# Optimization experiments

Measured on AMD Instinct MI355X. Metric: run time of the kernel, lower is better.

The kernel has to match this reference:

```python
import jax, jax.numpy as jnp
import numpy as np

B, N, DM, H = 2, 512, 1024, 16  # batch, seq, d_model, n_heads
DEPTHS = [1, 2, 4, 8]
LAM = 0.1  # lambda_distance


def setup_inputs() -> dict:
    key = jax.random.key(0)
    ks = jax.random.split(key, 2 + 5 * len(DEPTHS))
    inp = {
        "x": jax.random.normal(ks[0], (B, N, DM), jnp.float32),
        "depth_logits": jax.random.normal(ks[1], (len(DEPTHS),), jnp.float32),
    }
    j = 2
    for i, D in enumerate(DEPTHS):
        ds = DM // D
        r = max(1, D // 4)
        inp[f"pe{i}"] = jax.random.normal(ks[j], (N, D, ds), jnp.float32) * 0.02; j += 1
        inp[f"wqkv{i}"] = jax.random.normal(ks[j], (D, ds, 3 * ds), jnp.float32) / np.sqrt(ds); j += 1
        inp[f"wo{i}"] = jax.random.normal(ks[j], (DM, DM), jnp.float32) / np.sqrt(DM); j += 1
        inp[f"fu{i}"] = jax.random.normal(ks[j], (D, r), jnp.float32) / np.sqrt(r); j += 1
        inp[f"fv{i}"] = jax.random.normal(ks[j], (r, D), jnp.float32); j += 1
    return inp


def _ring_bias(n, lam, dtype):
    # toroidal (circular) distance bias on the sequence ring, normalized by N/2
    idx = jnp.arange(n)
    diff = jnp.abs(idx[:, None] - idx[None, :])
    ring = jnp.minimum(diff, n - diff).astype(dtype)
    return -lam * ring * (2.0 / n)  # [N, N]


def _toroidal_branch(x, pe, wqkv, wo, fu, fv):
    # x: [B, N, DM]; pe: [N, D, ds]; wqkv: [D, ds, 3ds]; wo: [DM, DM]; fu@fv: [D, D]
    b, n, dm = x.shape
    d_depth, ds, _ = wqkv.shape
    hd = ds // H
    xs = x.reshape(b, n, d_depth, ds) + pe[None]          # [B, N, D, ds]
    qkv = jnp.einsum('bnds,dse->bnde', xs, wqkv)          # per-depth-slice projection
    q, k, v = jnp.split(qkv, 3, axis=-1)
    q = q.reshape(b, n, d_depth, H, hd)
    k = k.reshape(b, n, d_depth, H, hd)
    v = v.reshape(b, n, d_depth, H, hd)
    bias = _ring_bias(n, LAM, x.dtype)
    scores = jnp.einsum('bndhe,bmdhe->bdhnm', q, k) / jnp.sqrt(jnp.asarray(hd, x.dtype))
    attn = jax.nn.softmax(scores + bias, axis=-1)          # [B, D, H, N, N]
    o = jnp.einsum('bdhnm,bmdhe->bndhe', attn, v).reshape(b, n, d_depth, ds)
    mix = fu @ fv                                          # low-rank depth fusion [D, D]
    fused = jnp.einsum('df,bnfs->bnds', mix, o).reshape(b, n, dm)
    return fused @ wo


def _forward(x, depth_logits, pe0, wqkv0, wo0, fu0, fv0, pe1, wqkv1, wo1, fu1, fv1,
             pe2, wqkv2, wo2, fu2, fv2, pe3, wqkv3, wo3, fu3, fv3):
    # inference-mode depth selection: hard one-hot at argmax (all branches still computed)
    w = jax.nn.one_hot(jnp.argmax(depth_logits), depth_logits.shape[0], dtype=x.dtype)
    params = [(pe0, wqkv0, wo0, fu0, fv0), (pe1, wqkv1, wo1, fu1, fv1),
              (pe2, wqkv2, wo2, fu2, fv2), (pe3, wqkv3, wo3, fu3, fv3)]
    out = jnp.zeros_like(x)
    for i, p in enumerate(params):
        out = out + w[i] * _toroidal_branch(x, *p)
    return out


def reference(x, depth_logits, pe0, wqkv0, wo0, fu0, fv0, pe1, wqkv1, wo1, fu1, fv1,
              pe2, wqkv2, wo2, fu2, fv2, pe3, wqkv3, wo3, fu3, fv3):
    return _forward(x, depth_logits, pe0, wqkv0, wo0, fu0, fv0, pe1, wqkv1, wo1, fu1, fv1,
                    pe2, wqkv2, wo2, fu2, fv2, pe3, wqkv3, wo3, fu3, fv3)
```

## Files before the change

### kernel.cpp

```cpp
#include <hip/hip_runtime.h>

#define B_   2
#define N_   512
#define DM_  1024
#define H_   16
#define LAM_ 0.1f

typedef __attribute__((ext_vector_type(8))) short bf16x8;
typedef __attribute__((ext_vector_type(4))) float f32x4;
typedef unsigned short ush;
struct ush4 { ush x, y, z, w; };

__device__ inline ush f2bf(float v) {
    union { float f; unsigned u; } c; c.f = v;
    unsigned r = c.u + 0x7FFF + ((c.u >> 16) & 1);
    return (ush)(r >> 16);
}
__device__ inline float bf2f(ush b) {
    union { float f; unsigned u; } c; c.u = ((unsigned)b) << 16; return c.f;
}
__device__ inline f32x4 mfma16(bf16x8 a, bf16x8 b, f32x4 c) {
    return __builtin_amdgcn_mfma_f32_16x16x32_bf16(a, b, c, 0, 0, 0);
}

__global__ void k_select(const float* __restrict__ logits, int* __restrict__ sel) {
    if (threadIdx.x == 0) {
        float best = logits[0]; int bi = 0;
        for (int i = 1; i < 4; ++i) { float v = logits[i]; if (v > best) { best = v; bi = i; } }
        *sel = bi;
    }
}

template<int D>
__device__ void prep_w_body(size_t i, const float* __restrict__ w,
                            ush* __restrict__ wh, ush* __restrict__ wl) {
    constexpr int ds = DM_ / D;
    constexpr size_t TOT = (size_t)D * ds * 3 * ds;
    if (i >= TOT) return;
    const int per = ds * 3 * ds;
    const int d = (int)(i / per), rem = (int)(i % per);
    const int s = rem / (3 * ds), e = rem % (3 * ds);
    const float v = w[i];
    const size_t o = (size_t)d * 3 * ds * ds + (size_t)e * ds + s;
    const ush h = f2bf(v);
    wh[o] = h; wl[o] = f2bf(v - bf2f(h));
}
__global__ __launch_bounds__(256) void k_prep(
        const int* __restrict__ sel, const float* __restrict__ x,
        const float* __restrict__ pe0, const float* __restrict__ pe1,
        const float* __restrict__ pe2, const float* __restrict__ pe3,
        const float* __restrict__ w0, const float* __restrict__ w1,
        const float* __restrict__ w2, const float* __restrict__ w3,
        const float* __restrict__ wo0, const float* __restrict__ wo1,
        const float* __restrict__ wo2, const float* __restrict__ wo3,
        ush* __restrict__ xh, ush* __restrict__ xl,
        ush* __restrict__ wqh, ush* __restrict__ wql,
        ush* __restrict__ woh, ush* __restrict__ wol) {
    const int s = *sel;
    const int bid = blockIdx.x, tid = threadIdx.x;
    if (bid < 4096) {
        const float* pe = (s == 0) ? pe0 : (s == 1) ? pe1 : (s == 2) ? pe2 : pe3;
        const size_t i = (size_t)bid * 256 + tid;
        const float v = x[i] + pe[i % ((size_t)N_ * DM_)];
        const ush h = f2bf(v);
        xh[i] = h; xl[i] = f2bf(v - bf2f(h));
    } else if (bid < 16384) {
        const size_t i = (size_t)(bid - 4096) * 256 + tid;
        switch (s) {
            case 0: prep_w_body<1>(i, w0, wqh, wql); break;
            case 1: prep_w_body<2>(i, w1, wqh, wql); break;
            case 2: prep_w_body<4>(i, w2, wqh, wql); break;
            case 3: prep_w_body<8>(i, w3, wqh, wql); break;
        }
    } else {
        const float* w = (s == 0) ? wo0 : (s == 1) ? wo1 : (s == 2) ? wo2 : wo3;
        const size_t i = (size_t)(bid - 16384) * 256 + tid;
        const int k = (int)(i / DM_), j = (int)(i % DM_);
        const float v = w[i];
        const size_t o = (size_t)j * DM_ + k;
        const ush h = f2bf(v);
        woh[o] = h; wol[o] = f2bf(v - bf2f(h));
    }
}

template<int KD>
__device__ void gemm_core(const ush* __restrict__ Ah, const ush* __restrict__ Al, int lda,
                          const ush* __restrict__ Bh, const ush* __restrict__ Bl, int ldb,
                          int row0, int col0, int tid, ush* lds, f32x4 acc[2][2]) {
    ush* lAh = lds; ush* lAl = lds + 2560; ush* lBh = lds + 5120; ush* lBl = lds + 7680;
    const int srow = tid >> 2, scg = tid & 3;
    const int lane = tid & 63, w = tid >> 6;
    const int wm = w >> 1, wn = w & 1;
    const int lr = lane & 15, lb = lane >> 4;

    for (int k0 = 0; k0 < KD; k0 += 32) {
        *(bf16x8*)&lAh[srow * 40 + scg * 8] =
            *(const bf16x8*)&Ah[(size_t)(row0 + srow) * lda + k0 + scg * 8];
        *(bf16x8*)&lAl[srow * 40 + scg * 8] =
            *(const bf16x8*)&Al[(size_t)(row0 + srow) * lda + k0 + scg * 8];
        *(bf16x8*)&lBh[srow * 40 + scg * 8] =
            *(const bf16x8*)&Bh[(size_t)(col0 + srow) * ldb + k0 + scg * 8];
        *(bf16x8*)&lBl[srow * 40 + scg * 8] =
            *(const bf16x8*)&Bl[(size_t)(col0 + srow) * ldb + k0 + scg * 8];
        __syncthreads();
        bf16x8 ah[2], al[2], bh[2], bl[2];
        #pragma unroll
        for (int mg = 0; mg < 2; ++mg) {
            const int r = wm * 32 + mg * 16 + lr;
            ah[mg] = *(const bf16x8*)&lAh[r * 40 + lb * 8];
            al[mg] = *(const bf16x8*)&lAl[r * 40 + lb * 8];
        }
        #pragma unroll
        for (int ng = 0; ng < 2; ++ng) {
            const int r = wn * 32 + ng * 16 + lr;
            bh[ng] = *(const bf16x8*)&lBh[r * 40 + lb * 8];
            bl[ng] = *(const bf16x8*)&lBl[r * 40 + lb * 8];
        }
        #pragma unroll
        for (int mg = 0; mg < 2; ++mg)
            #pragma unroll
            for (int ng = 0; ng < 2; ++ng) {
                acc[mg][ng] = mfma16(ah[mg], bh[ng], acc[mg][ng]);
                acc[mg][ng] = mfma16(al[mg], bh[ng], acc[mg][ng]);
                acc[mg][ng] = mfma16(ah[mg], bl[ng], acc[mg][ng]);
            }
        __syncthreads();
    }
}

template<int D>
__device__ void qkv_body(int bid, int tid,
                         const ush* __restrict__ xh, const ush* __restrict__ xl,
                         const ush* __restrict__ wh, const ush* __restrict__ wl,
                         ush* __restrict__ Qh, ush* __restrict__ Ql,
                         ush* __restrict__ Kh, ush* __restrict__ Kl,
                         ush* __restrict__ Vth, ush* __restrict__ Vtl, ush* lds) {
    constexpr int ds = DM_ / D;
    constexpr int hd = ds / H_;
    constexpr int nx = 3 * ds / 64;
    const int bx = bid % nx, by = (bid / nx) & 7, bz = bid / (nx * 8);
    const int b = bz / D, d = bz % D;
    const int row0 = by * 64, col0 = bx * 64;

    f32x4 acc[2][2] = {};
    gemm_core<ds>(xh + (size_t)b * N_ * DM_ + d * ds, xl + (size_t)b * N_ * DM_ + d * ds, DM_,
                  wh + (size_t)d * 3 * ds * ds, wl + (size_t)d * 3 * ds * ds, ds,
                  row0, col0, tid, lds, acc);

    const int lane = tid & 63, w = tid >> 6;
    const int wm = w >> 1, wn = w & 1;
    const int lr = lane & 15, lb = lane >> 4;
    #pragma unroll
    for (int mg = 0; mg < 2; ++mg)
        #pragma unroll
        for (int ng = 0; ng < 2; ++ng) {
            const int n0 = row0 + wm * 32 + mg * 16 + lb * 4;
            const int e  = col0 + wn * 32 + ng * 16 + lr;
            const int part = e / ds, ep = e % ds;
            const int h = ep / hd, t = ep % hd;
            const size_t head = ((size_t)b * D + d) * H_ + h;
            if (part == 2) {
                ush4 h4, l4;
                const float v0 = acc[mg][ng][0], v1 = acc[mg][ng][1];
                const float v2 = acc[mg][ng][2], v3 = acc[mg][ng][3];
                h4.x = f2bf(v0); l4.x = f2bf(v0 - bf2f(h4.x));
                h4.y = f2bf(v1); l4.y = f2bf(v1 - bf2f(h4.y));
                h4.z = f2bf(v2); l4.z = f2bf(v2 - bf2f(h4.z));
                h4.w = f2bf(v3); l4.w = f2bf(v3 - bf2f(h4.w));
                const size_t o = (head * hd + t) * N_ + n0;
                *(ush4*)&Vth[o] = h4;
                *(ush4*)&Vtl[o] = l4;
            } else {
                #pragma unroll
                for (int i = 0; i < 4; ++i) {
                    const size_t o = (head * N_ + n0 + i) * hd + t;
                    const float v = acc[mg][ng][i];
                    const ush hh = f2bf(v), ll = f2bf(v - bf2f(hh));
                    if (part == 0) { Qh[o] = hh; Ql[o] = ll; }
                    else           { Kh[o] = hh; Kl[o] = ll; }
                }
            }
        }
}
__global__ __launch_bounds__(256) void k_qkv(
        const int* __restrict__ sel,
        const ush* __restrict__ xh, const ush* __restrict__ xl,
        const ush* __restrict__ wh, const ush* __restrict__ wl,
        ush* __restrict__ Qh, ush* __restrict__ Ql,
        ush* __restrict__ Kh, ush* __restrict__ Kl,
        ush* __restrict__ Vth, ush* __restrict__ Vtl) {
    __shared__ ush lds[4 * 2560];
    const int bid = blockIdx.x, tid = threadIdx.x;
    switch (*sel) {
        case 0: qkv_body<1>(bid, tid, xh, xl, wh, wl, Qh, Ql, Kh, Kl, Vth, Vtl, lds); break;
        case 1: qkv_body<2>(bid, tid, xh, xl, wh, wl, Qh, Ql, Kh, Kl, Vth, Vtl, lds); break;
        case 2: qkv_body<4>(bid, tid, xh, xl, wh, wl, Qh, Ql, Kh, Kl, Vth, Vtl, lds); break;
        case 3: qkv_body<8>(bid, tid, xh, xl, wh, wl, Qh, Ql, Kh, Kl, Vth, Vtl, lds); break;
    }
}

template<int D>
__device__ void attn_body(int bid, int tid,
        const ush* __restrict__ Qh, const ush* __restrict__ Ql,
        const ush* __restrict__ Kh, const ush* __restrict__ Kl,
        const ush* __restrict__ Vth, const ush* __restrict__ Vtl,
        float* __restrict__ O, ush* P, float* redm, float* redl) {
    constexpr int ds = DM_ / D, hd = ds / H_;
    constexpr int CH = (hd >= 64) ? 2 : 1;
    constexpr int NT = (hd >= 16) ? hd / 16 : 1;
    constexpr int NHEAD = B_ * D * H_;
    constexpr int NB = NHEAD * 32;
    if (bid >= NB) return;
    const int bidr = (bid & 7) * (NB / 8) + (bid >> 3);
    const int head = bidr >> 5, qt = bidr & 31;
    const int h = head % H_, d = (head / H_) % D, b = head / (H_ * D);
    const int q0 = qt * 16;
    const size_t hb = (size_t)head * N_ * hd;
    const int lane = tid & 63, wk = tid >> 6;
    const int lr = lane & 15, lb = lane >> 4;
    const float L2E = 1.44269504f;
    const float SC  = rsqrtf((float)hd) * L2E;
    const float RB2 = LAM_ * (2.0f / N_) * L2E;
    const bf16x8 z8 = {0, 0, 0, 0, 0, 0, 0, 0};

    bf16x8 qah[CH], qal[CH];
    #pragma unroll
    for (int c = 0; c < CH; ++c) {
        const int k0 = c * 32 + lb * 8;
        bf16x8 vh = z8, vl = z8;
        if (k0 < hd) {
            const size_t o = hb + (size_t)(q0 + lr) * hd + k0;
            vh = *(const bf16x8*)&Qh[o];
            vl = *(const bf16x8*)&Ql[o];
        }
        qah[c] = vh; qal[c] = vl;
    }

    f32x4 s[8];
    #pragma unroll
    for (int t = 0; t < 8; ++t) {
        const int kj0 = wk * 128 + t * 16;
        f32x4 acc = {0.f, 0.f, 0.f, 0.f};
        #pragma unroll
        for (int c = 0; c < CH; ++c) {
            const int k0 = c * 32 + lb * 8;
            bf16x8 kh8 = z8, kl8 = z8;
            if (k0 < hd) {
                const size_t o = hb + (size_t)(kj0 + lr) * hd + k0;
                kh8 = *(const bf16x8*)&Kh[o];
                kl8 = *(const bf16x8*)&Kl[o];
            }
            acc = mfma16(qah[c], kh8, acc);
            acc = mfma16(qal[c], kh8, acc);
            acc = mfma16(qah[c], kl8, acc);
        }
        s[t] = acc;
    }

    float m4[4] = {-1e30f, -1e30f, -1e30f, -1e30f};
    #pragma unroll
    for (int t = 0; t < 8; ++t) {
        const int col = wk * 128 + t * 16 + lr;
        #pragma unroll
        for (int i = 0; i < 4; ++i) {
            const int rn = q0 + lb * 4 + i;
            int dd = rn - col; dd = dd < 0 ? -dd : dd;
            const int ring = (dd < N_ - dd) ? dd : (N_ - dd);
            const float v = s[t][i] * SC - RB2 * (float)ring;
            s[t][i] = v;
            m4[i] = fmaxf(m4[i], v);
        }
    }
    #pragma unroll
    for (int i = 0; i < 4; ++i) {
        m4[i] = fmaxf(m4[i], __shfl_xor(m4[i], 1));
        m4[i] = fmaxf(m4[i], __shfl_xor(m4[i], 2));
        m4[i] = fmaxf(m4[i], __shfl_xor(m4[i], 4));
        m4[i] = fmaxf(m4[i], __shfl_xor(m4[i], 8));
    }
    if (lr == 0) {
        #pragma unroll
        for (int i = 0; i < 4; ++i) redm[wk * 16 + lb * 4 + i] = m4[i];
    }

    ush* Pw = P + wk * 2048;
    float ls[4] = {0.f, 0.f, 0.f, 0.f};
    #pragma unroll
    for (int t = 0; t < 8; t += 2) {
        #pragma unroll
        for (int i = 0; i < 4; ++i) {
            const int row = lb * 4 + i;
            const float pe = exp2f(s[t][i] - m4[i]);
            const float po = exp2f(s[t + 1][i] - m4[i]);
            unsigned pk;
            asm("v_cvt_pk_bf16_f32 %0, %1, %2" : "=v"(pk) : "v"(pe), "v"(po));
            union { unsigned u; float f; } clo, chi;
            clo.u = pk << 16;
            chi.u = pk & 0xffff0000u;
            ls[i] += clo.f + chi.f;
            const int swz = (row & 7) << 4;
            const int offe = ((row << 8) + ((t * 16 + lr) << 1)) ^ swz;
            const int offo = ((row << 8) + (((t + 1) * 16 + lr) << 1)) ^ swz;
            *(ush*)((char*)Pw + offe) = (ush)pk;
            *(ush*)((char*)Pw + offo) = (ush)(pk >> 16);
        }
    }
    #pragma unroll
    for (int i = 0; i < 4; ++i) {
        ls[i] += __shfl_xor(ls[i], 1);
        ls[i] += __shfl_xor(ls[i], 2);
        ls[i] += __shfl_xor(ls[i], 4);
        ls[i] += __shfl_xor(ls[i], 8);
    }
    if (lr == 0) {
        #pragma unroll
        for (int i = 0; i < 4; ++i) redl[wk * 16 + lb * 4 + i] = ls[i];
    }

    f32x4 acc2[NT];
    #pragma unroll
    for (int tt = 0; tt < NT; ++tt) acc2[tt] = (f32x4){0.f, 0.f, 0.f, 0.f};
    #pragma unroll
    for (int jc = 0; jc < 4; ++jc) {
        int poff = ((lr << 8) + ((jc * 32 + lb * 8) << 1)) ^ ((lr & 7) << 4);
        const bf16x8 pa = *(const bf16x8*)((const char*)Pw + poff);
        #pragma unroll
        for (int tt = 0; tt < NT; ++tt) {
            const size_t o = hb + (size_t)(tt * 16 + lr) * N_ + wk * 128 + jc * 32 + lb * 8;
            const bf16x8 vh8 = *(const bf16x8*)&Vth[o];
            const bf16x8 vl8 = *(const bf16x8*)&Vtl[o];
            acc2[tt] = mfma16(pa, vh8, acc2[tt]);
            acc2[tt] = mfma16(pa, vl8, acc2[tt]);
        }
    }

    __syncthreads();
    float* res = (float*)P;
    if (wk != 0) {
        #pragma unroll
        for (int tt = 0; tt < NT; ++tt)
            #pragma unroll
            for (int i = 0; i < 4; ++i)
                res[((wk - 1) * NT + tt) * 256 + i * 64 + lane] = acc2[tt][i];
    }
    __syncthreads();
    if (wk == 0) {
        float scw[4][4], linv[4];
        #pragma unroll
        for (int i = 0; i < 4; ++i) {
            const int r = lb * 4 + i;
            const float mw0 = redm[r], mw1 = redm[16 + r];
            const float mw2 = redm[32 + r], mw3 = redm[48 + r];
            const float m = fmaxf(fmaxf(mw0, mw1), fmaxf(mw2, mw3));
            scw[i][0] = exp2f(mw0 - m); scw[i][1] = exp2f(mw1 - m);
            scw[i][2] = exp2f(mw2 - m); scw[i][3] = exp2f(mw3 - m);
            const float l = redl[r] * scw[i][0] + redl[16 + r] * scw[i][1]
                          + redl[32 + r] * scw[i][2] + redl[48 + r] * scw[i][3];
            linv[i] = 1.0f / l;
        }
        #pragma unroll
        for (int tt = 0; tt < NT; ++tt)
            #pragma unroll
            for (int i = 0; i < 4; ++i) {
                const float o = acc2[tt][i] * scw[i][0]
                    + res[(0 * NT + tt) * 256 + i * 64 + lane] * scw[i][1]
                    + res[(1 * NT + tt) * 256 + i * 64 + lane] * scw[i][2]
                    + res[(2 * NT + tt) * 256 + i * 64 + lane] * scw[i][3];
                const int rn = q0 + lb * 4 + i;
                const int tc = tt * 16 + lr;
                if (tc < hd)
                    O[((size_t)b * N_ + rn) * DM_ + d * ds + h * hd + tc] = o * linv[i];
            }
    }
}
__global__ __launch_bounds__(256) void k_attn(
        const int* __restrict__ sel,
        const ush* __restrict__ Qh, const ush* __restrict__ Ql,
        const ush* __restrict__ Kh, const ush* __restrict__ Kl,
        const ush* __restrict__ Vth, const ush* __restrict__ Vtl,
        float* __restrict__ O) {
    __shared__ __align__(16) ush P[4 * 16 * 128];
    __shared__ float redm[64], redl[64];
    const int bid = blockIdx.x, tid = threadIdx.x;
    switch (*sel) {
        case 0: attn_body<1>(bid, tid, Qh, Ql, Kh, Kl, Vth, Vtl, O, P, redm, redl); break;
        case 1: attn_body<2>(bid, tid, Qh, Ql, Kh, Kl, Vth, Vtl, O, P, redm, redl); break;
        case 2: attn_body<4>(bid, tid, Qh, Ql, Kh, Kl, Vth, Vtl, O, P, redm, redl); break;
        case 3: attn_body<8>(bid, tid, Qh, Ql, Kh, Kl, Vth, Vtl, O, P, redm, redl); break;
    }
}

template<int D>
__device__ void mix_body(int bid, int tid, const float* __restrict__ fu,
                         const float* __restrict__ fv, const float* __restrict__ O,
                         ush* __restrict__ Fh, ush* __restrict__ Fl, float* mixs) {
    constexpr int ds = DM_ / D;
    constexpr int R = (D / 4 > 0) ? (D / 4) : 1;
    if (tid < D * D) {
        const int d = tid / D, f = tid % D;
        float m = 0.f;
        #pragma unroll
        for (int rr = 0; rr < R; ++rr) m += fu[d * R + rr] * fv[rr * D + f];
        mixs[tid] = m;
    }
    __syncthreads();
    const size_t idx = (size_t)bid * 256 + tid;
    const int dm = (int)(idx % DM_);
    const size_t bn = idx / DM_;
    const int d = dm / ds, s0 = dm % ds;
    const float* Ob = O + bn * DM_ + s0;
    float acc = 0.f;
    #pragma unroll
    for (int f = 0; f < D; ++f) acc += mixs[d * D + f] * Ob[(size_t)f * ds];
    const ush hh = f2bf(acc);
    Fh[idx] = hh; Fl[idx] = f2bf(acc - bf2f(hh));
}
__global__ __launch_bounds__(256) void k_mix(
        const int* __restrict__ sel,
        const float* __restrict__ fu0, const float* __restrict__ fv0,
        const float* __restrict__ fu1, const float* __restrict__ fv1,
        const float* __restrict__ fu2, const float* __restrict__ fv2,
        const float* __restrict__ fu3, const float* __restrict__ fv3,
        const float* __restrict__ O, ush* __restrict__ Fh, ush* __restrict__ Fl) {
    __shared__ float mixs[64];
    const int bid = blockIdx.x, tid = threadIdx.x;
    switch (*sel) {
        case 0: mix_body<1>(bid, tid, fu0, fv0, O, Fh, Fl, mixs); break;
        case 1: mix_body<2>(bid, tid, fu1, fv1, O, Fh, Fl, mixs); break;
        case 2: mix_body<4>(bid, tid, fu2, fv2, O, Fh, Fl, mixs); break;
        case 3: mix_body<8>(bid, tid, fu3, fv3, O, Fh, Fl, mixs); break;
    }
}

__global__ __launch_bounds__(256) void k_wo(
        const ush* __restrict__ Fh, const ush* __restrict__ Fl,
        const ush* __restrict__ wh, const ush* __restrict__ wl,
        float* __restrict__ out) {
    __shared__ ush lds[4 * 2560];
    const int tid = threadIdx.x;
    const int bx = blockIdx.x % 16, by = blockIdx.x / 16;
    const int row0 = by * 64, col0 = bx * 64;
    f32x4 acc[2][2] = {};
    gemm_core<DM_>(Fh, Fl, DM_, wh, wl, DM_, row0, col0, tid, lds, acc);
    const int lane = tid & 63, w = tid >> 6;
    const int wm = w >> 1, wn = w & 1;
    const int lr = lane & 15, lb = lane >> 4;
    #pragma unroll
    for (int mg = 0; mg < 2; ++mg)
        #pragma unroll
        for (int ng = 0; ng < 2; ++ng)
            #pragma unroll
            for (int i = 0; i < 4; ++i) {
                const int r = row0 + wm * 32 + mg * 16 + lb * 4 + i;
                const int c = col0 + wn * 32 + ng * 16 + lr;
                out[(size_t)r * DM_ + c] = acc[mg][ng][i];
            }
}

extern "C" void kernel_launch(void* const* d_in, const int* in_sizes, int n_in,
                              void* d_out, int out_size, void* d_ws, size_t ws_size,
                              hipStream_t stream) {
    const float* x      = (const float*)d_in[0];
    const float* logits = (const float*)d_in[1];
    float* out = (float*)d_out;

    char* p = (char*)d_ws;
    int* sel = (int*)p; p += 256;
    const size_t MB = 1024 * 1024;
    ush* Qh = (ush*)p; p += 2 * MB;
    ush* Ql = (ush*)p; p += 2 * MB;
    ush* Kh = (ush*)p; p += 2 * MB;
    ush* Kl = (ush*)p; p += 2 * MB;
    ush* Vth = (ush*)p; p += 2 * MB + 65536;
    ush* Vtl = (ush*)p; p += 2 * MB + 65536;
    float* O = (float*)p; p += 4 * MB;
    ush* xh = (ush*)p; p += 2 * MB;
    ush* xl = (ush*)p; p += 2 * MB;
    ush* wqh = (ush*)p; p += 6 * MB;
    ush* wql = (ush*)p; p += 6 * MB;
    ush* woh = (ush*)p; p += 2 * MB;
    ush* wol = (ush*)p; p += 2 * MB;
    ush* Fh = xh, *Fl = xl;

    k_select<<<1, 64, 0, stream>>>(logits, sel);
    k_prep<<<dim3(20480), dim3(256), 0, stream>>>(
        sel, x,
        (const float*)d_in[2], (const float*)d_in[7],
        (const float*)d_in[12], (const float*)d_in[17],
        (const float*)d_in[3], (const float*)d_in[8],
        (const float*)d_in[13], (const float*)d_in[18],
        (const float*)d_in[4], (const float*)d_in[9],
        (const float*)d_in[14], (const float*)d_in[19],
        xh, xl, wqh, wql, woh, wol);
    k_qkv<<<dim3(768), dim3(256), 0, stream>>>(sel, xh, xl, wqh, wql,
                                               Qh, Ql, Kh, Kl, Vth, Vtl);
    k_attn<<<dim3(8192), dim3(256), 0, stream>>>(sel, Qh, Ql, Kh, Kl, Vth, Vtl, O);
    k_mix<<<dim3(B_ * N_ * DM_ / 256), dim3(256), 0, stream>>>(
        sel,
        (const float*)d_in[5],  (const float*)d_in[6],
        (const float*)d_in[10], (const float*)d_in[11],
        (const float*)d_in[15], (const float*)d_in[16],
        (const float*)d_in[20], (const float*)d_in[21],
        O, Fh, Fl);
    k_wo<<<dim3(256), dim3(256), 0, stream>>>(Fh, Fl, woh, wol, out);
}
```

Before: 109.2 us.

## Tile weight transposes via LDS, drop softmax max pass, retile output GEMM

```diff
diff --git a/kernel.cpp b/kernel.cpp
--- a/kernel.cpp
+++ b/kernel.cpp
@@ -10,6 +10,7 @@
 typedef __attribute__((ext_vector_type(4))) float f32x4;
 typedef unsigned short ush;
 struct ush4 { ush x, y, z, w; };
+struct uint2s { unsigned x, y; };
 
 __device__ inline ush f2bf(float v) {
     union { float f; unsigned u; } c; c.f = v;
@@ -32,18 +33,34 @@
 }
 
 template<int D>
-__device__ void prep_w_body(size_t i, const float* __restrict__ w,
-                            ush* __restrict__ wh, ush* __restrict__ wl) {
+__device__ void prep_wt_tile(int bT, int tid, const float* __restrict__ w,
+                             ush* __restrict__ wh, ush* __restrict__ wl,
+                             float (*lds)[65]) {
     constexpr int ds = DM_ / D;
-    constexpr size_t TOT = (size_t)D * ds * 3 * ds;
-    if (i >= TOT) return;
-    const int per = ds * 3 * ds;
-    const int d = (int)(i / per), rem = (int)(i % per);
-    const int s = rem / (3 * ds), e = rem % (3 * ds);
-    const float v = w[i];
-    const size_t o = (size_t)d * 3 * ds * ds + (size_t)e * ds + s;
-    const ush h = f2bf(v);
-    wh[o] = h; wl[o] = f2bf(v - bf2f(h));
+    constexpr int tpr = 3 * ds / 64;
+    constexpr int tpc = ds / 64;
+    constexpr int tpd = tpr * tpc;
+    if (bT >= D * tpd) return;
+    const int d = bT / tpd, rem = bT % tpd;
+    const int tr = rem / tpr, tc = rem % tpr;
+    const float* src = w + (size_t)d * ds * 3 * ds;
+    ush* dsth = wh + (size_t)d * 3 * ds * ds;
+    ush* dstl = wl + (size_t)d * 3 * ds * ds;
+    const int c = tid & 63, r0 = tid >> 6;
+    #pragma unroll
+    for (int j = 0; j < 16; ++j) {
+        const int r = j * 4 + r0;
+        lds[r][c] = src[(size_t)(tr * 64 + r) * (3 * ds) + tc * 64 + c];
+    }
+    __syncthreads();
+    #pragma unroll
+    for (int j = 0; j < 16; ++j) {
+        const int r = j * 4 + r0;
+        const float v = lds[c][r];
+        const size_t o = (size_t)(tc * 64 + r) * ds + tr * 64 + c;
+        const ush h = f2bf(v);
+        dsth[o] = h; dstl[o] = f2bf(v - bf2f(h));
+    }
 }
 __global__ __launch_bounds__(256) void k_prep(
         const int* __restrict__ sel, const float* __restrict__ x,
@@ -56,30 +73,49 @@
         ush* __restrict__ xh, ush* __restrict__ xl,
         ush* __restrict__ wqh, ush* __restrict__ wql,
         ush* __restrict__ woh, ush* __restrict__ wol) {
+    __shared__ float lds[64][65];
     const int s = *sel;
     const int bid = blockIdx.x, tid = threadIdx.x;
-    if (bid < 4096) {
+    if (bid < 1024) {
         const float* pe = (s == 0) ? pe0 : (s == 1) ? pe1 : (s == 2) ? pe2 : pe3;
-        const size_t i = (size_t)bid * 256 + tid;
-        const float v = x[i] + pe[i % ((size_t)N_ * DM_)];
-        const ush h = f2bf(v);
-        xh[i] = h; xl[i] = f2bf(v - bf2f(h));
-    } else if (bid < 16384) {
-        const size_t i = (size_t)(bid - 4096) * 256 + tid;
+        const size_t i0 = ((size_t)bid * 256 + tid) * 4;
+        const float4 xv = *(const float4*)&x[i0];
+        const float4 pv = *(const float4*)&pe[i0 & ((size_t)N_ * DM_ - 1)];
+        ush4 h4, l4;
+        float v;
+        v = xv.x + pv.x; h4.x = f2bf(v); l4.x = f2bf(v - bf2f(h4.x));
+        v = xv.y + pv.y; h4.y = f2bf(v); l4.y = f2bf(v - bf2f(h4.y));
+        v = xv.z + pv.z; h4.z = f2bf(v); l4.z = f2bf(v - bf2f(h4.z));
+        v = xv.w + pv.w; h4.w = f2bf(v); l4.w = f2bf(v - bf2f(h4.w));
+        *(ush4*)&xh[i0] = h4;
+        *(ush4*)&xl[i0] = l4;
+    } else if (bid < 1792) {
+        const int bT = bid - 1024;
         switch (s) {
-            case 0: prep_w_body<1>(i, w0, wqh, wql); break;
-            case 1: prep_w_body<2>(i, w1, wqh, wql); break;
-            case 2: prep_w_body<4>(i, w2, wqh, wql); break;
-            case 3: prep_w_body<8>(i, w3, wqh, wql); break;
+            case 0: prep_wt_tile<1>(bT, tid, w0, wqh, wql, lds); break;
+            case 1: prep_wt_tile<2>(bT, tid, w1, wqh, wql, lds); break;
+            case 2: prep_wt_tile<4>(bT, tid, w2, wqh, wql, lds); break;
+            case 3: prep_wt_tile<8>(bT, tid, w3, wqh, wql, lds); break;
         }
     } else {
         const float* w = (s == 0) ? wo0 : (s == 1) ? wo1 : (s == 2) ? wo2 : wo3;
-        const size_t i = (size_t)(bid - 16384) * 256 + tid;
-        const int k = (int)(i / DM_), j = (int)(i % DM_);
-        const float v = w[i];
-        const size_t o = (size_t)j * DM_ + k;
-        const ush h = f2bf(v);
-        woh[o] = h; wol[o] = f2bf(v - bf2f(h));
+        const int bT = bid - 1792;
+        const int tr = bT >> 4, tc = bT & 15;
+        const int c = tid & 63, r0 = tid >> 6;
+        #pragma unroll
+        for (int j = 0; j < 16; ++j) {
+            const int r = j * 4 + r0;
+            lds[r][c] = w[(size_t)(tr * 64 + r) * DM_ + tc * 64 + c];
+        }
+        __syncthreads();
+        #pragma unroll
+        for (int j = 0; j < 16; ++j) {
+            const int r = j * 4 + r0;
+            const float v = lds[c][r];
+            const size_t o = (size_t)(tc * 64 + r) * DM_ + tr * 64 + c;
+            const ush h = f2bf(v);
+            woh[o] = h; wol[o] = f2bf(v - bf2f(h));
+        }
     }
 }
 
@@ -204,7 +240,7 @@
         const ush* __restrict__ Qh, const ush* __restrict__ Ql,
         const ush* __restrict__ Kh, const ush* __restrict__ Kl,
         const ush* __restrict__ Vth, const ush* __restrict__ Vtl,
-        float* __restrict__ O, ush* P, float* redm, float* redl) {
+        float* __restrict__ O, ush* P, float* redl) {
     constexpr int ds = DM_ / D, hd = ds / H_;
     constexpr int CH = (hd >= 64) ? 2 : 1;
     constexpr int NT = (hd >= 16) ? hd / 16 : 1;
@@ -250,72 +286,40 @@
                 kh8 = *(const bf16x8*)&Kh[o];
                 kl8 = *(const bf16x8*)&Kl[o];
             }
-            acc = mfma16(qah[c], kh8, acc);
-            acc = mfma16(qal[c], kh8, acc);
-            acc = mfma16(qah[c], kl8, acc);
+            acc = mfma16(kh8, qah[c], acc);
+            acc = mfma16(kl8, qah[c], acc);
+            acc = mfma16(kh8, qal[c], acc);
         }
         s[t] = acc;
     }
 
-    float m4[4] = {-1e30f, -1e30f, -1e30f, -1e30f};
+    ush* Pw = P + wk * 2048;
+    const int q = q0 + lr;
+    float ls = 0.f;
     #pragma unroll
     for (int t = 0; t < 8; ++t) {
-        const int col = wk * 128 + t * 16 + lr;
+        const int kbase = wk * 128 + t * 16 + lb * 4;
+        float p[4];
         #pragma unroll
         for (int i = 0; i < 4; ++i) {
-            const int rn = q0 + lb * 4 + i;
-            int dd = rn - col; dd = dd < 0 ? -dd : dd;
+            int dd = q - (kbase + i); dd = dd < 0 ? -dd : dd;
             const int ring = (dd < N_ - dd) ? dd : (N_ - dd);
-            const float v = s[t][i] * SC - RB2 * (float)ring;
-            s[t][i] = v;
-            m4[i] = fmaxf(m4[i], v);
-        }
-    }
-    #pragma unroll
-    for (int i = 0; i < 4; ++i) {
-        m4[i] = fmaxf(m4[i], __shfl_xor(m4[i], 1));
-        m4[i] = fmaxf(m4[i], __shfl_xor(m4[i], 2));
-        m4[i] = fmaxf(m4[i], __shfl_xor(m4[i], 4));
-        m4[i] = fmaxf(m4[i], __shfl_xor(m4[i], 8));
-    }
-    if (lr == 0) {
-        #pragma unroll
-        for (int i = 0; i < 4; ++i) redm[wk * 16 + lb * 4 + i] = m4[i];
-    }
-
-    ush* Pw = P + wk * 2048;
-    float ls[4] = {0.f, 0.f, 0.f, 0.f};
-    #pragma unroll
-    for (int t = 0; t < 8; t += 2) {
-        #pragma unroll
-        for (int i = 0; i < 4; ++i) {
-            const int row = lb * 4 + i;
-            const float pe = exp2f(s[t][i] - m4[i]);
-            const float po = exp2f(s[t + 1][i] - m4[i]);
-            unsigned pk;
-            asm("v_cvt_pk_bf16_f32 %0, %1, %2" : "=v"(pk) : "v"(pe), "v"(po));
-            union { unsigned u; float f; } clo, chi;
-            clo.u = pk << 16;
-            chi.u = pk & 0xffff0000u;
-            ls[i] += clo.f + chi.f;
-            const int swz = (row & 7) << 4;
-            const int offe = ((row << 8) + ((t * 16 + lr) << 1)) ^ swz;
-            const int offo = ((row << 8) + (((t + 1) * 16 + lr) << 1)) ^ swz;
-            *(ush*)((char*)Pw + offe) = (ush)pk;
-            *(ush*)((char*)Pw + offo) = (ush)(pk >> 16);
-        }
-    }
-    #pragma unroll
-    for (int i = 0; i < 4; ++i) {
-        ls[i] += __shfl_xor(ls[i], 1);
-        ls[i] += __shfl_xor(ls[i], 2);
-        ls[i] += __shfl_xor(ls[i], 4);
-        ls[i] += __shfl_xor(ls[i], 8);
-    }
-    if (lr == 0) {
-        #pragma unroll
-        for (int i = 0; i < 4; ++i) redl[wk * 16 + lb * 4 + i] = ls[i];
-    }
+            p[i] = exp2f(s[t][i] * SC - RB2 * (float)ring);
+        }
+        unsigned pk0, pk1;
+        asm("v_cvt_pk_bf16_f32 %0, %1, %2" : "=v"(pk0) : "v"(p[0]), "v"(p[1]));
+        asm("v_cvt_pk_bf16_f32 %0, %1, %2" : "=v"(pk1) : "v"(p[2]), "v"(p[3]));
+        union { unsigned u; float f; } c0, c1, c2, c3;
+        c0.u = pk0 << 16; c1.u = pk0 & 0xffff0000u;
+        c2.u = pk1 << 16; c3.u = pk1 & 0xffff0000u;
+        ls += (c0.f + c1.f) + (c2.f + c3.f);
+        const int off = ((lr << 8) + ((t * 16 + lb * 4) << 1)) ^ ((lr & 7) << 4);
+        uint2s pv; pv.x = pk0; pv.y = pk1;
+        *(uint2s*)((char*)Pw + off) = pv;
+    }
+    ls += __shfl_xor(ls, 16);
+    ls += __shfl_xor(ls, 32);
+    if (lb == 0) redl[wk * 16 + lr] = ls;
 
     f32x4 acc2[NT];
     #pragma unroll
@@ -345,27 +349,20 @@
     }
     __syncthreads();
     if (wk == 0) {
-        float scw[4][4], linv[4];
+        float linv[4];
         #pragma unroll
         for (int i = 0; i < 4; ++i) {
             const int r = lb * 4 + i;
-            const float mw0 = redm[r], mw1 = redm[16 + r];
-            const float mw2 = redm[32 + r], mw3 = redm[48 + r];
-            const float m = fmaxf(fmaxf(mw0, mw1), fmaxf(mw2, mw3));
-            scw[i][0] = exp2f(mw0 - m); scw[i][1] = exp2f(mw1 - m);
-            scw[i][2] = exp2f(mw2 - m); scw[i][3] = exp2f(mw3 - m);
-            const float l = redl[r] * scw[i][0] + redl[16 + r] * scw[i][1]
-                          + redl[32 + r] * scw[i][2] + redl[48 + r] * scw[i][3];
-            linv[i] = 1.0f / l;
+            linv[i] = 1.0f / (redl[r] + redl[16 + r] + redl[32 + r] + redl[48 + r]);
         }
         #pragma unroll
         for (int tt = 0; tt < NT; ++tt)
             #pragma unroll
             for (int i = 0; i < 4; ++i) {
-                const float o = acc2[tt][i] * scw[i][0]
-                    + res[(0 * NT + tt) * 256 + i * 64 + lane] * scw[i][1]
-                    + res[(1 * NT + tt) * 256 + i * 64 + lane] * scw[i][2]
-                    + res[(2 * NT + tt) * 256 + i * 64 + lane] * scw[i][3];
+                const float o = acc2[tt][i]
+                    + res[(0 * NT + tt) * 256 + i * 64 + lane]
+                    + res[(1 * NT + tt) * 256 + i * 64 + lane]
+                    + res[(2 * NT + tt) * 256 + i * 64 + lane];
                 const int rn = q0 + lb * 4 + i;
                 const int tc = tt * 16 + lr;
                 if (tc < hd)
@@ -380,13 +377,13 @@
         const ush* __restrict__ Vth, const ush* __restrict__ Vtl,
         float* __restrict__ O) {
     __shared__ __align__(16) ush P[4 * 16 * 128];
-    __shared__ float redm[64], redl[64];
+    __shared__ float redl[64];
     const int bid = blockIdx.x, tid = threadIdx.x;
     switch (*sel) {
-        case 0: attn_body<1>(bid, tid, Qh, Ql, Kh, Kl, Vth, Vtl, O, P, redm, redl); break;
-        case 1: attn_body<2>(bid, tid, Qh, Ql, Kh, Kl, Vth, Vtl, O, P, redm, redl); break;
-        case 2: attn_body<4>(bid, tid, Qh, Ql, Kh, Kl, Vth, Vtl, O, P, redm, redl); break;
-        case 3: attn_body<8>(bid, tid, Qh, Ql, Kh, Kl, Vth, Vtl, O, P, redm, redl); break;
+        case 0: attn_body<1>(bid, tid, Qh, Ql, Kh, Kl, Vth, Vtl, O, P, redl); break;
+        case 1: attn_body<2>(bid, tid, Qh, Ql, Kh, Kl, Vth, Vtl, O, P, redl); break;
+        case 2: attn_body<4>(bid, tid, Qh, Ql, Kh, Kl, Vth, Vtl, O, P, redl); break;
+        case 3: attn_body<8>(bid, tid, Qh, Ql, Kh, Kl, Vth, Vtl, O, P, redl); break;
     }
 }
 
@@ -436,25 +433,54 @@
         const ush* __restrict__ Fh, const ush* __restrict__ Fl,
         const ush* __restrict__ wh, const ush* __restrict__ wl,
         float* __restrict__ out) {
-    __shared__ ush lds[4 * 2560];
+    __shared__ ush lA[2][32 * 40];
+    __shared__ ush lB[2][64 * 40];
     const int tid = threadIdx.x;
-    const int bx = blockIdx.x % 16, by = blockIdx.x / 16;
-    const int row0 = by * 64, col0 = bx * 64;
-    f32x4 acc[2][2] = {};
-    gemm_core<DM_>(Fh, Fl, DM_, wh, wl, DM_, row0, col0, tid, lds, acc);
+    const int bx = blockIdx.x & 15, by = blockIdx.x >> 4;
+    const int row0 = by * 32, col0 = bx * 64;
     const int lane = tid & 63, w = tid >> 6;
-    const int wm = w >> 1, wn = w & 1;
+    const int wq = w >> 1, wn = w & 1;
     const int lr = lane & 15, lb = lane >> 4;
-    #pragma unroll
-    for (int mg = 0; mg < 2; ++mg)
-        #pragma unroll
-        for (int ng = 0; ng < 2; ++ng)
-            #pragma unroll
-            for (int i = 0; i < 4; ++i) {
-                const int r = row0 + wm * 32 + mg * 16 + lb * 4 + i;
-                const int c = col0 + wn * 32 + ng * 16 + lr;
-                out[(size_t)r * DM_ + c] = acc[mg][ng][i];
-            }
+    f32x4 acc[2] = {};
+
+    for (int k0 = 0; k0 < DM_; k0 += 32) {
+        {
+            const int half = tid >> 7, t2 = tid & 127;
+            const int srow = t2 >> 2, scg = t2 & 3;
+            const ush* src = half ? Fl : Fh;
+            *(bf16x8*)&lA[half][srow * 40 + scg * 8] =
+                *(const bf16x8*)&src[(size_t)(row0 + srow) * DM_ + k0 + scg * 8];
+        }
+        {
+            const int srow = tid >> 2, scg = tid & 3;
+            *(bf16x8*)&lB[0][srow * 40 + scg * 8] =
+                *(const bf16x8*)&wh[(size_t)(col0 + srow) * DM_ + k0 + scg * 8];
+            *(bf16x8*)&lB[1][srow * 40 + scg * 8] =
+                *(const bf16x8*)&wl[(size_t)(col0 + srow) * DM_ + k0 + scg * 8];
+        }
+        __syncthreads();
+        const int ar = wq * 16 + lr;
+        const bf16x8 ah = *(const bf16x8*)&lA[0][ar * 40 + lb * 8];
+        const bf16x8 al = *(const bf16x8*)&lA[1][ar * 40 + lb * 8];
+        #pragma unroll
+        for (int ng = 0; ng < 2; ++ng) {
+            const int br = wn * 32 + ng * 16 + lr;
+            const bf16x8 bh = *(const bf16x8*)&lB[0][br * 40 + lb * 8];
+            const bf16x8 bl = *(const bf16x8*)&lB[1][br * 40 + lb * 8];
+            acc[ng] = mfma16(ah, bh, acc[ng]);
+            acc[ng] = mfma16(al, bh, acc[ng]);
+            acc[ng] = mfma16(ah, bl, acc[ng]);
+        }
+        __syncthreads();
+    }
+    #pragma unroll
+    for (int ng = 0; ng < 2; ++ng)
+        #pragma unroll
+        for (int i = 0; i < 4; ++i) {
+            const int r = row0 + wq * 16 + lb * 4 + i;
+            const int c = col0 + wn * 32 + ng * 16 + lr;
+            out[(size_t)r * DM_ + c] = acc[ng][i];
+        }
 }
 
 extern "C" void kernel_launch(void* const* d_in, const int* in_sizes, int n_in,
@@ -483,7 +509,7 @@
     ush* Fh = xh, *Fl = xl;
 
     k_select<<<1, 64, 0, stream>>>(logits, sel);
-    k_prep<<<dim3(20480), dim3(256), 0, stream>>>(
+    k_prep<<<dim3(2048), dim3(256), 0, stream>>>(
         sel, x,
         (const float*)d_in[2], (const float*)d_in[7],
         (const float*)d_in[12], (const float*)d_in[17],
@@ -502,5 +528,5 @@
         (const float*)d_in[15], (const float*)d_in[16],
         (const float*)d_in[20], (const float*)d_in[21],
         O, Fh, Fl);
-    k_wo<<<dim3(256), dim3(256), 0, stream>>>(Fh, Fl, woh, wol, out);
-}
+    k_wo<<<dim3(512), dim3(256), 0, stream>>>(Fh, Fl, woh, wol, out);
+}
```

Measured after the change: 89.58 us. 1.22x faster.
